# Optimization experiments

Measured on AMD Instinct MI355X. Metric: run time of the kernel, lower is better.

Reference implementation:

```python
import jax, jax.numpy as jnp
import numpy as np

N, E = 50000, 400000
HID, HT = 128, 128
HEADS, C = 4, 128  # TransformerConv heads=4, out_channels=hidden_X


def setup_inputs() -> dict:
    key = jax.random.key(0)
    ks = jax.random.split(key, 16)
    s = lambda k, shape, fan: jax.random.normal(k, shape, jnp.float32) / np.sqrt(fan)
    return {
        "edge_index": jax.random.randint(ks[0], (2, E), 0, N, dtype=jnp.int32),
        "h_X": jax.random.normal(ks[1], (N, HID), jnp.float32),
        "h_t": jax.random.normal(ks[2], (1, HT), jnp.float32),
        # TransformerConv params: lin_query/key/value: (HID -> HEADS*C), lin_skip: (HID -> C)
        "Wq": s(ks[3], (HID, HEADS * C), HID), "bq": jnp.zeros((HEADS * C,), jnp.float32),
        "Wk": s(ks[4], (HID, HEADS * C), HID), "bk": jnp.zeros((HEADS * C,), jnp.float32),
        "Wv": s(ks[5], (HID, HEADS * C), HID), "bv": jnp.zeros((HEADS * C,), jnp.float32),
        "Wskip": s(ks[6], (HID, C), HID), "bskip": jnp.zeros((C,), jnp.float32),
        # update_X: Linear(HID+HT -> HID), LayerNorm(HID)
        "Wup": s(ks[7], (HID + HT, HID), HID + HT), "bup": jnp.zeros((HID,), jnp.float32),
        "gamma": jnp.ones((HID,), jnp.float32), "beta": jnp.zeros((HID,), jnp.float32),
    }


def transformer_conv(h_X, edge_index, Wq, bq, Wk, bk, Wv, bv, Wskip, bskip):
    n = h_X.shape[0]
    src, dst = edge_index[0], edge_index[1]  # messages flow src -> dst
    q = (h_X @ Wq + bq).reshape(n, HEADS, C)
    k = (h_X @ Wk + bk).reshape(n, HEADS, C)
    v = (h_X @ Wv + bv).reshape(n, HEADS, C)
    # per-edge attention scores [E, H]
    score = jnp.einsum('ehc,ehc->eh', q[dst], k[src]) / np.sqrt(C)
    # segment softmax over incoming edges of each destination node
    m = jax.ops.segment_max(score, dst, num_segments=n)          # [N, H]
    ex = jnp.exp(score - m[dst])                                 # [E, H]
    denom = jax.ops.segment_sum(ex, dst, num_segments=n)        # [N, H]
    alpha = ex / denom[dst]                                      # [E, H]
    agg = jax.ops.segment_sum(alpha[..., None] * v[src], dst, num_segments=n)  # [N, H, C]
    out = agg.mean(axis=1)                                       # concat=False -> mean over heads
    return out + h_X @ Wskip + bskip                             # root_weight=True


def reference(edge_index, h_X, h_t, Wq, bq, Wk, bk, Wv, bv, Wskip, bskip,
              Wup, bup, gamma, beta):
    n = h_X.shape[0]
    h_att = transformer_conv(h_X, edge_index, Wq, bq, Wk, bk, Wv, bv, Wskip, bskip)
    h_t_exp = jnp.broadcast_to(h_t, (n, h_t.shape[1]))
    h = jnp.concatenate([h_att, h_t_exp], axis=1)
    h = jax.nn.relu(h @ Wup + bup)
    # LayerNorm (eps=1e-5); Dropout is identity in eval
    mu = h.mean(axis=-1, keepdims=True)
    var = ((h - mu) ** 2).mean(axis=-1, keepdims=True)
    return (h - mu) / jnp.sqrt(var + 1e-5) * gamma + beta
```

## Files before the change

kernel.cpp:

```cpp
#include <hip/hip_runtime.h>

typedef unsigned short u16;
typedef unsigned int   u32;

#define HID   128
#define HEADS 4
#define CH    128
#define HC    512
#define UT    32

typedef __bf16 bf16x8v __attribute__((ext_vector_type(8)));
typedef float  f32x4v  __attribute__((ext_vector_type(4)));
union FragU { uint4 u; bf16x8v b; };

static __device__ __forceinline__ float bf2f(u16 u) {
  union { u32 u; float f; } x;
  x.u = ((u32)u) << 16;
  return x.f;
}
static __device__ __forceinline__ u16 f2bf(float f) {
  union { float f; u32 u; } x;
  x.f = f;
  u32 r = x.u + 0x7fffu + ((x.u >> 16) & 1u);
  return (u16)(r >> 16);
}

static __device__ __forceinline__ void unpack8(uint4 raw, float* dst) {
  dst[0] = bf2f((u16)(raw.x & 0xffffu));
  dst[1] = bf2f((u16)(raw.x >> 16));
  dst[2] = bf2f((u16)(raw.y & 0xffffu));
  dst[3] = bf2f((u16)(raw.y >> 16));
  dst[4] = bf2f((u16)(raw.z & 0xffffu));
  dst[5] = bf2f((u16)(raw.z >> 16));
  dst[6] = bf2f((u16)(raw.w & 0xffffu));
  dst[7] = bf2f((u16)(raw.w >> 16));
}

__global__ void zero_kernel(int* p, int n) {
  int i = blockIdx.x * 256 + threadIdx.x;
  if (i < n) p[i] = 0;
}

__global__ void hist_kernel(const int* dst_idx, int* deg, int E) {
  int e = blockIdx.x * 256 + threadIdx.x;
  if (e < E) atomicAdd(&deg[dst_idx[e]], 1);
}

__global__ void blocksum_kernel(const int* deg, int* bsums, int n) {
  __shared__ int buf[256];
  int i = blockIdx.x * 256 + threadIdx.x;
  int v = 0;
  if (i < n) v = deg[i];
  buf[threadIdx.x] = v;
  __syncthreads();
  for (int off = 128; off > 0; off >>= 1) {
    if (threadIdx.x < off) buf[threadIdx.x] += buf[threadIdx.x + off];
    __syncthreads();
  }
  if (threadIdx.x == 0) bsums[blockIdx.x] = buf[0];
}

__global__ void scanb_kernel(const int* bsums, int* boffs, int nb) {
  __shared__ int buf[256];
  __shared__ int carry_s;
  int tid = threadIdx.x;
  if (tid == 0) carry_s = 0;
  __syncthreads();
  for (int base = 0; base < nb; base += 256) {
    int i = base + tid;
    int v = 0;
    if (i < nb) v = bsums[i];
    buf[tid] = v;
    __syncthreads();
    for (int off = 1; off < 256; off <<= 1) {
      int t = 0;
      if (tid >= off) t = buf[tid - off];
      __syncthreads();
      buf[tid] += t;
      __syncthreads();
    }
    int incl = buf[tid] + carry_s;
    if (i < nb) boffs[i] = incl - v;
    __syncthreads();
    if (tid == 255) carry_s = incl;
    __syncthreads();
  }
}

__global__ void scanfinal_kernel(const int* deg, const int* boffs,
                                 int* row_ptr, int* cursor, int n) {
  __shared__ int buf[256];
  int tid = threadIdx.x;
  int i = blockIdx.x * 256 + tid;
  int v = 0;
  if (i < n) v = deg[i];
  buf[tid] = v;
  __syncthreads();
  for (int off = 1; off < 256; off <<= 1) {
    int t = 0;
    if (tid >= off) t = buf[tid - off];
    __syncthreads();
    buf[tid] += t;
    __syncthreads();
  }
  int incl = buf[tid] + boffs[blockIdx.x];
  if (i < n) {
    row_ptr[i + 1] = incl;
    cursor[i] = incl - v;
  }
  if (i == 0) row_ptr[0] = 0;
}

__global__ void scatter_kernel(const int* src_idx, const int* dst_idx,
                               int* cursor, int* col, int E) {
  int e = blockIdx.x * 256 + threadIdx.x;
  if (e < E) {
    int pos = atomicAdd(&cursor[dst_idx[e]], 1);
    col[pos] = src_idx[e];
  }
}

__global__ void packH_kernel(const float* __restrict__ hX,
                             u16* __restrict__ hpack, int N, int total) {
  int i = blockIdx.x * 256 + threadIdx.x;
  if (i >= total) return;
  int j = i & 7;
  int lane = (i >> 3) & 63;
  int kc = (i >> 9) & 3;
  int ntile = i >> 11;
  int node = ntile * 16 + (lane & 15);
  int k = kc * 32 + (lane >> 4) * 8 + j;
  float v = (node < N) ? hX[(size_t)node * HID + k] : 0.f;
  hpack[i] = f2bf(v);
}

__global__ void packW_kernel(const float* __restrict__ WA,
                             const float* __restrict__ WB, int colsA, int ldA,
                             int ldB, u16* __restrict__ Wp, int total) {
  int i = blockIdx.x * 256 + threadIdx.x;
  if (i >= total) return;
  int j = i & 7;
  int lane = (i >> 3) & 63;
  int kc = (i >> 9) & 3;
  int ct = i >> 11;
  int n = ct * 16 + (lane & 15);
  int k = kc * 32 + (lane >> 4) * 8 + j;
  float w = (n < colsA) ? WA[(size_t)k * ldA + n]
                        : WB[(size_t)k * ldB + (n - colsA)];
  Wp[i] = f2bf(w);
}

__global__ __launch_bounds__(256) void mfma_proj_kernel(
    const u16* __restrict__ hpack, const u16* __restrict__ Wp,
    const float* __restrict__ biasLo, const float* __restrict__ biasHi,
    u16* __restrict__ outLo, u16* __restrict__ outHiB,
    float* __restrict__ outHiF, int hiIsF32, int N) {
  int t = threadIdx.x;
  int wv = t >> 6;
  int L = t & 63;
  int ct = blockIdx.y * 4 + wv;
  int nt0 = blockIdx.x * 4;

  f32x4v acc[4];
  for (int mt = 0; mt < 4; ++mt) acc[mt] = (f32x4v){0.f, 0.f, 0.f, 0.f};

  const u16* wb = Wp + (size_t)ct * 2048;
  const u16* hb = hpack + (size_t)nt0 * 2048;

  for (int kc = 0; kc < 4; ++kc) {
    FragU bf;
    bf.u = *(const uint4*)(wb + kc * 512 + L * 8);
    for (int mt = 0; mt < 4; ++mt) {
      FragU af;
      af.u = *(const uint4*)(hb + mt * 2048 + kc * 512 + L * 8);
      acc[mt] =
          __builtin_amdgcn_mfma_f32_16x16x32_bf16(af.b, bf.b, acc[mt], 0, 0, 0);
    }
  }

  int colq = L & 15;
  int quad = L >> 4;
  int n = ct * 16 + colq;
  float bias = (n < 512) ? biasLo[n] : biasHi[n - 512];
  for (int mt = 0; mt < 4; ++mt) {
    for (int rg = 0; rg < 4; ++rg) {
      int node = (nt0 + mt) * 16 + quad * 4 + rg;
      if (node < N) {
        float val = acc[mt][rg] + bias;
        if (n < 512) {
          outLo[(size_t)node * HC + n] = f2bf(val);
        } else if (hiIsF32) {
          outHiF[(size_t)node * HID + (n - 512)] = val;
        } else {
          outHiB[(size_t)node * HC + (n - 512)] = f2bf(val);
        }
      }
    }
  }
}

__global__ void fused_attn_kernel(const u16* __restrict__ qb,
                                  const u16* __restrict__ kb,
                                  const u16* __restrict__ vb,
                                  const int* __restrict__ row_ptr,
                                  const int* __restrict__ col_src,
                                  float* out, int N) {
  int node = blockIdx.x * 4 + (threadIdx.x >> 6);
  if (node >= N) return;
  int lane = threadIdx.x & 63;
  int head = lane >> 4;
  int r = lane & 15;
  int foff = head * CH + r * 8;
  const float sscale = 0.08838834764831845f;

  float qf[8];
  unpack8(*(const uint4*)(qb + (size_t)node * HC + foff), qf);

  float m = -3.402823466e38f;
  float l = 0.f;
  float acc[8];
  for (int j = 0; j < 8; ++j) acc[j] = 0.f;

  int e0 = row_ptr[node];
  int e1 = row_ptr[node + 1];
  int e = e0;
  for (; e + 2 <= e1; e += 2) {
    int s0 = col_src[e];
    int s1 = col_src[e + 1];
    uint4 k0 = *(const uint4*)(kb + (size_t)s0 * HC + foff);
    uint4 k1 = *(const uint4*)(kb + (size_t)s1 * HC + foff);
    uint4 v0 = *(const uint4*)(vb + (size_t)s0 * HC + foff);
    uint4 v1 = *(const uint4*)(vb + (size_t)s1 * HC + foff);
    float k0f[8], k1f[8];
    unpack8(k0, k0f);
    unpack8(k1, k1f);
    float p0 = 0.f, p1 = 0.f;
    for (int j = 0; j < 8; ++j) {
      p0 = fmaf(k0f[j], qf[j], p0);
      p1 = fmaf(k1f[j], qf[j], p1);
    }
    p0 += __shfl_xor(p0, 1);
    p1 += __shfl_xor(p1, 1);
    p0 += __shfl_xor(p0, 2);
    p1 += __shfl_xor(p1, 2);
    p0 += __shfl_xor(p0, 4);
    p1 += __shfl_xor(p1, 4);
    p0 += __shfl_xor(p0, 8);
    p1 += __shfl_xor(p1, 8);
    float sc0 = p0 * sscale;
    float sc1 = p1 * sscale;
    float mnew = fmaxf(m, fmaxf(sc0, sc1));
    float so = __expf(m - mnew);
    float pe0 = __expf(sc0 - mnew);
    float pe1 = __expf(sc1 - mnew);
    l = l * so + pe0 + pe1;
    float v0f[8], v1f[8];
    unpack8(v0, v0f);
    unpack8(v1, v1f);
    for (int j = 0; j < 8; ++j)
      acc[j] = fmaf(acc[j], so, fmaf(pe0, v0f[j], pe1 * v1f[j]));
    m = mnew;
  }
  if (e < e1) {
    int s0 = col_src[e];
    uint4 k0 = *(const uint4*)(kb + (size_t)s0 * HC + foff);
    uint4 v0 = *(const uint4*)(vb + (size_t)s0 * HC + foff);
    float k0f[8];
    unpack8(k0, k0f);
    float p0 = 0.f;
    for (int j = 0; j < 8; ++j) p0 = fmaf(k0f[j], qf[j], p0);
    p0 += __shfl_xor(p0, 1);
    p0 += __shfl_xor(p0, 2);
    p0 += __shfl_xor(p0, 4);
    p0 += __shfl_xor(p0, 8);
    float sc0 = p0 * sscale;
    float mnew = fmaxf(m, sc0);
    float so = __expf(m - mnew);
    float pe0 = __expf(sc0 - mnew);
    l = l * so + pe0;
    float v0f[8];
    unpack8(v0, v0f);
    for (int j = 0; j < 8; ++j) acc[j] = fmaf(acc[j], so, pe0 * v0f[j]);
    m = mnew;
  }

  float inv = 0.f;
  if (l > 0.f) inv = 1.0f / l;
  float val[8];
  for (int j = 0; j < 8; ++j) {
    float x = acc[j] * inv;
    x += __shfl_xor(x, 16);
    x += __shfl_xor(x, 32);
    val[j] = x * 0.25f;
  }

  if (head == 0) {
    float* p = out + (size_t)node * HID + r * 8;
    float4 a = *(const float4*)(p);
    float4 b = *(const float4*)(p + 4);
    a.x += val[0]; a.y += val[1]; a.z += val[2]; a.w += val[3];
    b.x += val[4]; b.y += val[5]; b.z += val[6]; b.w += val[7];
    *(float4*)(p) = a;
    *(float4*)(p + 4) = b;
  }
}

__global__ void score_kernel(const u16* qb, const u16* kb, const int* row_ptr,
                             const int* col_src, float* scores, int N) {
  int node = blockIdx.x * 4 + (threadIdx.x >> 6);
  if (node >= N) return;
  int lane = threadIdx.x & 63;
  int head = lane >> 4;
  int r = lane & 15;
  int foff = head * CH + r * 8;

  float qf[8];
  unpack8(*(const uint4*)(qb + (size_t)node * HC + foff), qf);

  int e0 = row_ptr[node];
  int e1 = row_ptr[node + 1];
  for (int e = e0; e < e1; ++e) {
    int s = col_src[e];
    uint4 raw = *(const uint4*)(kb + (size_t)s * HC + foff);
    float kf[8];
    unpack8(raw, kf);
    float p = 0.f;
    for (int j = 0; j < 8; ++j) p = fmaf(kf[j], qf[j], p);
    p += __shfl_xor(p, 1);
    p += __shfl_xor(p, 2);
    p += __shfl_xor(p, 4);
    p += __shfl_xor(p, 8);
    if (r == 0) scores[(size_t)e * HEADS + head] = p * 0.08838834764831845f;
  }
}

__global__ void attn_kernel(const float* scores, const u16* vb,
                            const int* row_ptr, const int* col_src,
                            float* out, int N) {
  int node = blockIdx.x * 4 + (threadIdx.x >> 6);
  if (node >= N) return;
  int lane = threadIdx.x & 63;
  int head = lane >> 4;
  int r = lane & 15;
  int foff = head * CH + r * 8;

  float m = -3.402823466e38f;
  float l = 0.f;
  float acc[8];
  for (int j = 0; j < 8; ++j) acc[j] = 0.f;

  int e0 = row_ptr[node];
  int e1 = row_ptr[node + 1];
  for (int e = e0; e < e1; ++e) {
    float sc = scores[(size_t)e * HEADS + head];
    int s = col_src[e];
    uint4 raw = *(const uint4*)(vb + (size_t)s * HC + foff);
    float vf[8];
    unpack8(raw, vf);
    float mnew = fmaxf(m, sc);
    float scale = __expf(m - mnew);
    float pe = __expf(sc - mnew);
    l = l * scale + pe;
    for (int j = 0; j < 8; ++j) acc[j] = fmaf(acc[j], scale, pe * vf[j]);
    m = mnew;
  }

  float inv = 0.f;
  if (l > 0.f) inv = 1.0f / l;
  float val[8];
  for (int j = 0; j < 8; ++j) {
    float x = acc[j] * inv;
    x += __shfl_xor(x, 16);
    x += __shfl_xor(x, 32);
    val[j] = x * 0.25f;
  }

  if (head == 0) {
    float* p = out + (size_t)node * HID + r * 8;
    float4 a = *(const float4*)(p);
    float4 b = *(const float4*)(p + 4);
    a.x += val[0]; a.y += val[1]; a.z += val[2]; a.w += val[3];
    b.x += val[4]; b.y += val[5]; b.z += val[6]; b.w += val[7];
    *(float4*)(p) = a;
    *(float4*)(p + 4) = b;
  }
}

__global__ void cvec_kernel(const float* h_t, const float* Wup,
                            const float* bup, float* cvec) {
  int c = threadIdx.x;
  float acc = bup[c];
  for (int k = 0; k < 128; ++k)
    acc = fmaf(h_t[k], Wup[(size_t)(128 + k) * 128 + c], acc);
  cvec[c] = acc;
}

__global__ __launch_bounds__(256) void ATTLayer_19396072308956_kernel(
    float* out, const float* __restrict__ Wup, const float* __restrict__ cvec,
    const float* __restrict__ gamma, const float* __restrict__ beta, int N) {
  __shared__ float Wl[64 * 128];
  __shared__ float Hl[UT * 128];
  int t = threadIdx.x;
  int n0 = blockIdx.x * UT;

  for (int i = t * 4; i < UT * 128; i += 1024) {
    int node = n0 + (i >> 7);
    float4 v;
    if (node < N) {
      v = *(const float4*)(out + (size_t)node * HID + (i & 127));
    } else {
      v.x = 0.f; v.y = 0.f; v.z = 0.f; v.w = 0.f;
    }
    *(float4*)(Hl + i) = v;
  }

  int wv = t >> 6;
  int r = t & 63;
  int c0 = 2 * r;
  float2 cv = *(const float2*)(cvec + c0);
  float a0[8];
  float a1[8];
  for (int j = 0; j < 8; ++j) {
    a0[j] = cv.x;
    a1[j] = cv.y;
  }

  for (int ph = 0; ph < 2; ++ph) {
    __syncthreads();
    for (int i = t * 4; i < 64 * 128; i += 1024) {
      *(float4*)(Wl + i) = *(const float4*)(Wup + (size_t)ph * 64 * 128 + i);
    }
    __syncthreads();
    const float* hbase = Hl + (wv * 8) * 128 + ph * 64;
#pragma unroll 8
    for (int k = 0; k < 64; ++k) {
      float2 w2 = *(const float2*)(Wl + k * 128 + c0);
      for (int j = 0; j < 8; ++j) {
        float h = hbase[j * 128 + k];
        a0[j] = fmaf(h, w2.x, a0[j]);
        a1[j] = fmaf(h, w2.y, a1[j]);
      }
    }
  }

  float2 g = *(const float2*)(gamma + c0);
  float2 b = *(const float2*)(beta + c0);
  for (int j = 0; j < 8; ++j) {
    int node = n0 + wv * 8 + j;
    float r0 = fmaxf(a0[j], 0.f);
    float r1 = fmaxf(a1[j], 0.f);
    float s = r0 + r1;
    for (int msk = 1; msk < 64; msk <<= 1) s += __shfl_xor(s, msk);
    float mean = s * (1.0f / 128.0f);
    float d0 = r0 - mean;
    float d1 = r1 - mean;
    float sq = d0 * d0 + d1 * d1;
    for (int msk = 1; msk < 64; msk <<= 1) sq += __shfl_xor(sq, msk);
    float rstd = rsqrtf(sq * (1.0f / 128.0f) + 1e-5f);
    if (node < N) {
      float2 o;
      o.x = d0 * rstd * g.x + b.x;
      o.y = d1 * rstd * g.y + b.y;
      *(float2*)(out + (size_t)node * HID + c0) = o;
    }
  }
}

extern "C" void kernel_launch(void* const* d_in, const int* in_sizes, int n_in,
                              void* d_out, int out_size, void* d_ws,
                              size_t ws_size, hipStream_t stream) {
  (void)n_in;
  (void)out_size;

  const int* edge_index = (const int*)d_in[0];
  const float* hX    = (const float*)d_in[1];
  const float* h_t   = (const float*)d_in[2];
  const float* Wq    = (const float*)d_in[3];
  const float* bq    = (const float*)d_in[4];
  const float* Wk    = (const float*)d_in[5];
  const float* bk    = (const float*)d_in[6];
  const float* Wv    = (const float*)d_in[7];
  const float* bv    = (const float*)d_in[8];
  const float* Wskip = (const float*)d_in[9];
  const float* bskip = (const float*)d_in[10];
  const float* Wup   = (const float*)d_in[11];
  const float* bup   = (const float*)d_in[12];
  const float* gamma = (const float*)d_in[13];
  const float* beta  = (const float*)d_in[14];

  const int E = in_sizes[0] / 2;
  const int N = in_sizes[1] / HID;
  const int* src_idx = edge_index;
  const int* dst_idx = edge_index + E;
  const int NB = (N + 255) / 256;
  const int NTILES = (N + 15) / 16;
  const int NTILES4 = ((NTILES + 3) / 4) * 4;

  char* w = (char*)d_ws;
  size_t off = 0;
  float* cvec = (float*)(w + off);
  off += 256 * 4;
  int* deg = (int*)(w + off);
  off += ((size_t)N * 4 + 255) / 256 * 256;
  int* row_ptr = (int*)(w + off);
  off += ((size_t)(N + 1) * 4 + 255) / 256 * 256;
  int* cursor = (int*)(w + off);
  off += ((size_t)N * 4 + 255) / 256 * 256;
  int* bsums = (int*)(w + off);
  off += ((size_t)NB * 4 + 255) / 256 * 256;
  int* boffs = (int*)(w + off);
  off += ((size_t)NB * 4 + 255) / 256 * 256;
  int* col = (int*)(w + off);
  off += ((size_t)E * 4 + 255) / 256 * 256;
  float* scores = (float*)(w + off);
  off += ((size_t)E * HEADS * 4 + 255) / 256 * 256;
  u16* hpack = (u16*)(w + off);
  off += ((size_t)NTILES4 * 2048 * 2 + 255) / 256 * 256;
  u16* Wp1 = (u16*)(w + off);
  off += ((size_t)128 * 1024 * 2 + 255) / 256 * 256;
  u16* Wp2 = (u16*)(w + off);
  off += ((size_t)128 * 640 * 2 + 255) / 256 * 256;
  u16* bigA = (u16*)(w + off);
  off += ((size_t)N * HC * 2 + 255) / 256 * 256;
  u16* bigB = (u16*)(w + off);
  off += ((size_t)N * HC * 2 + 255) / 256 * 256;
  u16* bigC = (u16*)(w + off);
  size_t off_fused = off + ((size_t)N * HC * 2 + 255) / 256 * 256;
  const int use_fused = (ws_size >= off_fused) ? 1 : 0;

  float* out = (float*)d_out;

  zero_kernel<<<NB, 256, 0, stream>>>(deg, N);
  hist_kernel<<<(E + 255) / 256, 256, 0, stream>>>(dst_idx, deg, E);
  blocksum_kernel<<<NB, 256, 0, stream>>>(deg, bsums, N);
  scanb_kernel<<<1, 256, 0, stream>>>(bsums, boffs, NB);
  scanfinal_kernel<<<NB, 256, 0, stream>>>(deg, boffs, row_ptr, cursor, N);
  scatter_kernel<<<(E + 255) / 256, 256, 0, stream>>>(src_idx, dst_idx, cursor,
                                                      col, E);

  int totH = NTILES4 * 2048;
  packH_kernel<<<(totH + 255) / 256, 256, 0, stream>>>(hX, hpack, N, totH);
  packW_kernel<<<(128 * 1024 + 255) / 256, 256, 0, stream>>>(
      Wq, Wk, 512, HC, HC, Wp1, 128 * 1024);
  packW_kernel<<<(128 * 640 + 255) / 256, 256, 0, stream>>>(
      Wv, Wskip, 512, HC, HID, Wp2, 128 * 640);

  cvec_kernel<<<1, 128, 0, stream>>>(h_t, Wup, bup, cvec);

  mfma_proj_kernel<<<dim3(NTILES4 / 4, 16), 256, 0, stream>>>(
      hpack, Wp1, bq, bk, bigA, bigB, (float*)nullptr, 0, N);

  if (use_fused) {
    mfma_proj_kernel<<<dim3(NTILES4 / 4, 10), 256, 0, stream>>>(
        hpack, Wp2, bv, bskip, bigC, (u16*)nullptr, out, 1, N);
    fused_attn_kernel<<<(N + 3) / 4, 256, 0, stream>>>(bigA, bigB, bigC,
                                                       row_ptr, col, out, N);
  } else {
    score_kernel<<<(N + 3) / 4, 256, 0, stream>>>(bigA, bigB, row_ptr, col,
                                                  scores, N);
    mfma_proj_kernel<<<dim3(NTILES4 / 4, 10), 256, 0, stream>>>(
        hpack, Wp2, bv, bskip, bigA, (u16*)nullptr, out, 1, N);
    attn_kernel<<<(N + 3) / 4, 256, 0, stream>>>(scores, bigA, row_ptr, col,
                                                 out, N);
  }

  ATTLayer_19396072308956_kernel<<<(N + UT - 1) / UT, 256, 0, stream>>>(
      out, Wup, cvec, gamma, beta, N);
}
```

Measured before the change: 447.9 us.

## Merge projection GEMMs into one launch and software-pipeline edge gathers in attention

The two weight-pack kernels and the two MFMA projection launches (Q/K and V/skip) are merged into one packing kernel and a single 26-column-tile projection launch that routes outputs to the q, k, v and skip buffers. The fused attention kernel now prefetches the next pair of neighbor K/V rows while it processes the current pair, and gets a launch_bounds occupancy hint. The unfused score/attn fallback and its workspace gating are removed, so the code assumes the workspace is large enough. This cuts launch overhead and hides gather latency, at the cost of more live registers in the attention loop.

New measurement: 456.7 us. Within noise of the previous version (+2.0%).

```diff
diff --git a/kernel.cpp b/kernel.cpp
--- a/kernel.cpp
+++ b/kernel.cpp
@@ -34,6 +34,42 @@
   dst[5] = bf2f((u16)(raw.z >> 16));
   dst[6] = bf2f((u16)(raw.w & 0xffffu));
   dst[7] = bf2f((u16)(raw.w >> 16));
+}
+
+static __device__ __forceinline__ void attn_pair(uint4 k0, uint4 k1, uint4 v0,
+                                                 uint4 v1, const float* qf,
+                                                 float& m, float& l,
+                                                 float* acc) {
+  const float sscale = 0.08838834764831845f;
+  float k0f[8], k1f[8];
+  unpack8(k0, k0f);
+  unpack8(k1, k1f);
+  float p0 = 0.f, p1 = 0.f;
+  for (int j = 0; j < 8; ++j) {
+    p0 = fmaf(k0f[j], qf[j], p0);
+    p1 = fmaf(k1f[j], qf[j], p1);
+  }
+  p0 += __shfl_xor(p0, 1);
+  p1 += __shfl_xor(p1, 1);
+  p0 += __shfl_xor(p0, 2);
+  p1 += __shfl_xor(p1, 2);
+  p0 += __shfl_xor(p0, 4);
+  p1 += __shfl_xor(p1, 4);
+  p0 += __shfl_xor(p0, 8);
+  p1 += __shfl_xor(p1, 8);
+  float sc0 = p0 * sscale;
+  float sc1 = p1 * sscale;
+  float mnew = fmaxf(m, fmaxf(sc0, sc1));
+  float so = __expf(m - mnew);
+  float pe0 = __expf(sc0 - mnew);
+  float pe1 = __expf(sc1 - mnew);
+  l = l * so + pe0 + pe1;
+  float v0f[8], v1f[8];
+  unpack8(v0, v0f);
+  unpack8(v1, v1f);
+  for (int j = 0; j < 8; ++j)
+    acc[j] = fmaf(acc[j], so, fmaf(pe0, v0f[j], pe1 * v1f[j]));
+  m = mnew;
 }
 
 __global__ void zero_kernel(int* p, int n) {
@@ -134,9 +170,11 @@
   hpack[i] = f2bf(v);
 }
 
-__global__ void packW_kernel(const float* __restrict__ WA,
-                             const float* __restrict__ WB, int colsA, int ldA,
-                             int ldB, u16* __restrict__ Wp, int total) {
+__global__ void packW4_kernel(const float* __restrict__ Wq,
+                              const float* __restrict__ Wk,
+                              const float* __restrict__ Wv,
+                              const float* __restrict__ Wsk,
+                              u16* __restrict__ Wp, int total) {
   int i = blockIdx.x * 256 + threadIdx.x;
   if (i >= total) return;
   int j = i & 7;
@@ -145,16 +183,20 @@
   int ct = i >> 11;
   int n = ct * 16 + (lane & 15);
   int k = kc * 32 + (lane >> 4) * 8 + j;
-  float w = (n < colsA) ? WA[(size_t)k * ldA + n]
-                        : WB[(size_t)k * ldB + (n - colsA)];
+  float w;
+  if (n < 512) w = Wq[(size_t)k * HC + n];
+  else if (n < 1024) w = Wk[(size_t)k * HC + (n - 512)];
+  else if (n < 1536) w = Wv[(size_t)k * HC + (n - 1024)];
+  else w = Wsk[(size_t)k * HID + (n - 1536)];
   Wp[i] = f2bf(w);
 }
 
 __global__ __launch_bounds__(256) void mfma_proj_kernel(
     const u16* __restrict__ hpack, const u16* __restrict__ Wp,
-    const float* __restrict__ biasLo, const float* __restrict__ biasHi,
-    u16* __restrict__ outLo, u16* __restrict__ outHiB,
-    float* __restrict__ outHiF, int hiIsF32, int N) {
+    const float* __restrict__ bq, const float* __restrict__ bk,
+    const float* __restrict__ bv, const float* __restrict__ bsk,
+    u16* __restrict__ qb, u16* __restrict__ kbuf, u16* __restrict__ vbuf,
+    float* __restrict__ skipf, int N) {
   int t = threadIdx.x;
   int wv = t >> 6;
   int L = t & 63;
@@ -181,37 +223,45 @@
   int colq = L & 15;
   int quad = L >> 4;
   int n = ct * 16 + colq;
-  float bias = (n < 512) ? biasLo[n] : biasHi[n - 512];
+  u16* outB;
+  const float* bias;
+  int nl;
+  int isF32 = 0;
+  if (n < 512) {
+    outB = qb; bias = bq; nl = n;
+  } else if (n < 1024) {
+    outB = kbuf; bias = bk; nl = n - 512;
+  } else if (n < 1536) {
+    outB = vbuf; bias = bv; nl = n - 1024;
+  } else {
+    outB = (u16*)skipf; bias = bsk; nl = n - 1536; isF32 = 1;
+  }
+  float bval = bias[nl];
   for (int mt = 0; mt < 4; ++mt) {
     for (int rg = 0; rg < 4; ++rg) {
       int node = (nt0 + mt) * 16 + quad * 4 + rg;
       if (node < N) {
-        float val = acc[mt][rg] + bias;
-        if (n < 512) {
-          outLo[(size_t)node * HC + n] = f2bf(val);
-        } else if (hiIsF32) {
-          outHiF[(size_t)node * HID + (n - 512)] = val;
+        float val = acc[mt][rg] + bval;
+        if (isF32) {
+          skipf[(size_t)node * HID + nl] = val;
         } else {
-          outHiB[(size_t)node * HC + (n - 512)] = f2bf(val);
+          outB[(size_t)node * HC + nl] = f2bf(val);
         }
       }
     }
   }
 }
 
-__global__ void fused_attn_kernel(const u16* __restrict__ qb,
-                                  const u16* __restrict__ kb,
-                                  const u16* __restrict__ vb,
-                                  const int* __restrict__ row_ptr,
-                                  const int* __restrict__ col_src,
-                                  float* out, int N) {
+__global__ __launch_bounds__(256, 8) void fused_attn_kernel(
+    const u16* __restrict__ qb, const u16* __restrict__ kb,
+    const u16* __restrict__ vb, const int* __restrict__ row_ptr,
+    const int* __restrict__ col_src, float* out, int N) {
   int node = blockIdx.x * 4 + (threadIdx.x >> 6);
   if (node >= N) return;
   int lane = threadIdx.x & 63;
   int head = lane >> 4;
   int r = lane & 15;
   int foff = head * CH + r * 8;
-  const float sscale = 0.08838834764831845f;
 
   float qf[8];
   unpack8(*(const uint4*)(qb + (size_t)node * HC + foff), qf);
@@ -224,44 +274,35 @@
   int e0 = row_ptr[node];
   int e1 = row_ptr[node + 1];
   int e = e0;
-  for (; e + 2 <= e1; e += 2) {
+
+  uint4 ka, kc_, va, vc_;
+  if (e + 2 <= e1) {
     int s0 = col_src[e];
     int s1 = col_src[e + 1];
-    uint4 k0 = *(const uint4*)(kb + (size_t)s0 * HC + foff);
-    uint4 k1 = *(const uint4*)(kb + (size_t)s1 * HC + foff);
-    uint4 v0 = *(const uint4*)(vb + (size_t)s0 * HC + foff);
-    uint4 v1 = *(const uint4*)(vb + (size_t)s1 * HC + foff);
-    float k0f[8], k1f[8];
-    unpack8(k0, k0f);
-    unpack8(k1, k1f);
-    float p0 = 0.f, p1 = 0.f;
-    for (int j = 0; j < 8; ++j) {
-      p0 = fmaf(k0f[j], qf[j], p0);
-      p1 = fmaf(k1f[j], qf[j], p1);
-    }
-    p0 += __shfl_xor(p0, 1);
-    p1 += __shfl_xor(p1, 1);
-    p0 += __shfl_xor(p0, 2);
-    p1 += __shfl_xor(p1, 2);
-    p0 += __shfl_xor(p0, 4);
-    p1 += __shfl_xor(p1, 4);
-    p0 += __shfl_xor(p0, 8);
-    p1 += __shfl_xor(p1, 8);
-    float sc0 = p0 * sscale;
-    float sc1 = p1 * sscale;
-    float mnew = fmaxf(m, fmaxf(sc0, sc1));
-    float so = __expf(m - mnew);
-    float pe0 = __expf(sc0 - mnew);
-    float pe1 = __expf(sc1 - mnew);
-    l = l * so + pe0 + pe1;
-    float v0f[8], v1f[8];
-    unpack8(v0, v0f);
-    unpack8(v1, v1f);
-    for (int j = 0; j < 8; ++j)
-      acc[j] = fmaf(acc[j], so, fmaf(pe0, v0f[j], pe1 * v1f[j]));
-    m = mnew;
+    ka = *(const uint4*)(kb + (size_t)s0 * HC + foff);
+    kc_ = *(const uint4*)(kb + (size_t)s1 * HC + foff);
+    va = *(const uint4*)(vb + (size_t)s0 * HC + foff);
+    vc_ = *(const uint4*)(vb + (size_t)s1 * HC + foff);
+  }
+  for (; e + 4 <= e1; e += 2) {
+    int s2 = col_src[e + 2];
+    int s3 = col_src[e + 3];
+    uint4 nk0 = *(const uint4*)(kb + (size_t)s2 * HC + foff);
+    uint4 nk1 = *(const uint4*)(kb + (size_t)s3 * HC + foff);
+    uint4 nv0 = *(const uint4*)(vb + (size_t)s2 * HC + foff);
+    uint4 nv1 = *(const uint4*)(vb + (size_t)s3 * HC + foff);
+    attn_pair(ka, kc_, va, vc_, qf, m, l, acc);
+    ka = nk0;
+    kc_ = nk1;
+    va = nv0;
+    vc_ = nv1;
+  }
+  if (e + 2 <= e1) {
+    attn_pair(ka, kc_, va, vc_, qf, m, l, acc);
+    e += 2;
   }
   if (e < e1) {
+    const float sscale = 0.08838834764831845f;
     int s0 = col_src[e];
     uint4 k0 = *(const uint4*)(kb + (size_t)s0 * HC + foff);
     uint4 v0 = *(const uint4*)(vb + (size_t)s0 * HC + foff);
@@ -305,87 +346,6 @@
   }
 }
 
-__global__ void score_kernel(const u16* qb, const u16* kb, const int* row_ptr,
-                             const int* col_src, float* scores, int N) {
-  int node = blockIdx.x * 4 + (threadIdx.x >> 6);
-  if (node >= N) return;
-  int lane = threadIdx.x & 63;
-  int head = lane >> 4;
-  int r = lane & 15;
-  int foff = head * CH + r * 8;
-
-  float qf[8];
-  unpack8(*(const uint4*)(qb + (size_t)node * HC + foff), qf);
-
-  int e0 = row_ptr[node];
-  int e1 = row_ptr[node + 1];
-  for (int e = e0; e < e1; ++e) {
-    int s = col_src[e];
-    uint4 raw = *(const uint4*)(kb + (size_t)s * HC + foff);
-    float kf[8];
-    unpack8(raw, kf);
-    float p = 0.f;
-    for (int j = 0; j < 8; ++j) p = fmaf(kf[j], qf[j], p);
-    p += __shfl_xor(p, 1);
-    p += __shfl_xor(p, 2);
-    p += __shfl_xor(p, 4);
-    p += __shfl_xor(p, 8);
-    if (r == 0) scores[(size_t)e * HEADS + head] = p * 0.08838834764831845f;
-  }
-}
-
-__global__ void attn_kernel(const float* scores, const u16* vb,
-                            const int* row_ptr, const int* col_src,
-                            float* out, int N) {
-  int node = blockIdx.x * 4 + (threadIdx.x >> 6);
-  if (node >= N) return;
-  int lane = threadIdx.x & 63;
-  int head = lane >> 4;
-  int r = lane & 15;
-  int foff = head * CH + r * 8;
-
-  float m = -3.402823466e38f;
-  float l = 0.f;
-  float acc[8];
-  for (int j = 0; j < 8; ++j) acc[j] = 0.f;
-
-  int e0 = row_ptr[node];
-  int e1 = row_ptr[node + 1];
-  for (int e = e0; e < e1; ++e) {
-    float sc = scores[(size_t)e * HEADS + head];
-    int s = col_src[e];
-    uint4 raw = *(const uint4*)(vb + (size_t)s * HC + foff);
-    float vf[8];
-    unpack8(raw, vf);
-    float mnew = fmaxf(m, sc);
-    float scale = __expf(m - mnew);
-    float pe = __expf(sc - mnew);
-    l = l * scale + pe;
-    for (int j = 0; j < 8; ++j) acc[j] = fmaf(acc[j], scale, pe * vf[j]);
-    m = mnew;
-  }
-
-  float inv = 0.f;
-  if (l > 0.f) inv = 1.0f / l;
-  float val[8];
-  for (int j = 0; j < 8; ++j) {
-    float x = acc[j] * inv;
-    x += __shfl_xor(x, 16);
-    x += __shfl_xor(x, 32);
-    val[j] = x * 0.25f;
-  }
-
-  if (head == 0) {
-    float* p = out + (size_t)node * HID + r * 8;
-    float4 a = *(const float4*)(p);
-    float4 b = *(const float4*)(p + 4);
-    a.x += val[0]; a.y += val[1]; a.z += val[2]; a.w += val[3];
-    b.x += val[4]; b.y += val[5]; b.z += val[6]; b.w += val[7];
-    *(float4*)(p) = a;
-    *(float4*)(p + 4) = b;
-  }
-}
-
 __global__ void cvec_kernel(const float* h_t, const float* Wup,
                             const float* bup, float* cvec) {
   int c = threadIdx.x;
@@ -471,6 +431,7 @@
                               size_t ws_size, hipStream_t stream) {
   (void)n_in;
   (void)out_size;
+  (void)ws_size;
 
   const int* edge_index = (const int*)d_in[0];
   const float* hX    = (const float*)d_in[1];
@@ -512,21 +473,16 @@
   off += ((size_t)NB * 4 + 255) / 256 * 256;
   int* col = (int*)(w + off);
   off += ((size_t)E * 4 + 255) / 256 * 256;
-  float* scores = (float*)(w + off);
-  off += ((size_t)E * HEADS * 4 + 255) / 256 * 256;
   u16* hpack = (u16*)(w + off);
   off += ((size_t)NTILES4 * 2048 * 2 + 255) / 256 * 256;
-  u16* Wp1 = (u16*)(w + off);
-  off += ((size_t)128 * 1024 * 2 + 255) / 256 * 256;
-  u16* Wp2 = (u16*)(w + off);
-  off += ((size_t)128 * 640 * 2 + 255) / 256 * 256;
+  u16* Wp = (u16*)(w + off);
+  off += ((size_t)128 * 1664 * 2 + 255) / 256 * 256;
   u16* bigA = (u16*)(w + off);
   off += ((size_t)N * HC * 2 + 255) / 256 * 256;
   u16* bigB = (u16*)(w + off);
   off += ((size_t)N * HC * 2 + 255) / 256 * 256;
   u16* bigC = (u16*)(w + off);
-  size_t off_fused = off + ((size_t)N * HC * 2 + 255) / 256 * 256;
-  const int use_fused = (ws_size >= off_fused) ? 1 : 0;
+  off += ((size_t)N * HC * 2 + 255) / 256 * 256;
 
   float* out = (float*)d_out;
 
@@ -540,29 +496,16 @@
 
   int totH = NTILES4 * 2048;
   packH_kernel<<<(totH + 255) / 256, 256, 0, stream>>>(hX, hpack, N, totH);
-  packW_kernel<<<(128 * 1024 + 255) / 256, 256, 0, stream>>>(
-      Wq, Wk, 512, HC, HC, Wp1, 128 * 1024);
-  packW_kernel<<<(128 * 640 + 255) / 256, 256, 0, stream>>>(
-      Wv, Wskip, 512, HC, HID, Wp2, 128 * 640);
+  packW4_kernel<<<(128 * 1664 + 255) / 256, 256, 0, stream>>>(
+      Wq, Wk, Wv, Wskip, Wp, 128 * 1664);
 
   cvec_kernel<<<1, 128, 0, stream>>>(h_t, Wup, bup, cvec);
 
-  mfma_proj_kernel<<<dim3(NTILES4 / 4, 16), 256, 0, stream>>>(
-      hpack, Wp1, bq, bk, bigA, bigB, (float*)nullptr, 0, N);
-
-  if (use_fused) {
-    mfma_proj_kernel<<<dim3(NTILES4 / 4, 10), 256, 0, stream>>>(
-        hpack, Wp2, bv, bskip, bigC, (u16*)nullptr, out, 1, N);
-    fused_attn_kernel<<<(N + 3) / 4, 256, 0, stream>>>(bigA, bigB, bigC,
-                                                       row_ptr, col, out, N);
-  } else {
-    score_kernel<<<(N + 3) / 4, 256, 0, stream>>>(bigA, bigB, row_ptr, col,
-                                                  scores, N);
-    mfma_proj_kernel<<<dim3(NTILES4 / 4, 10), 256, 0, stream>>>(
-        hpack, Wp2, bv, bskip, bigA, (u16*)nullptr, out, 1, N);
-    attn_kernel<<<(N + 3) / 4, 256, 0, stream>>>(scores, bigA, row_ptr, col,
-                                                 out, N);
-  }
+  mfma_proj_kernel<<<dim3(NTILES4 / 4, 26), 256, 0, stream>>>(
+      hpack, Wp, bq, bk, bv, bskip, bigA, bigB, bigC, out, N);
+
+  fused_attn_kernel<<<(N + 3) / 4, 256, 0, stream>>>(bigA, bigB, bigC, row_ptr,
+                                                     col, out, N);
 
   ATTLayer_19396072308956_kernel<<<(N + UT - 1) / UT, 256, 0, stream>>>(
       out, Wup, cvec, gamma, beta, N);
```
